# Performance work log

Hardware: AMD Instinct MI355X
Metric: run time of the kernel (lower is better)

## Reference

```python
import jax, jax.numpy as jnp
import numpy as np

K = 8               # top-k frequencies
PRED_LEN = 96       # prediction_length
LOW_FREQ = 1        # low_frequency cutoff (drops DC)


def setup_inputs() -> dict:
    key = jax.random.key(0)
    x = jax.random.normal(key, (32, 2048, 64), dtype=jnp.float32)
    return {"x": x}


def reference(x):
    b, t, d = x.shape
    x_freq = jnp.fft.rfft(x, axis=1)                 # (b, t//2+1, d) complex
    freqs = jnp.fft.rfftfreq(t).astype(x.dtype)
    if t % 2 == 0:
        x_freq = x_freq[:, LOW_FREQ:-1]              # drop DC and Nyquist
        f = freqs[LOW_FREQ:-1]
    else:
        x_freq = x_freq[:, LOW_FREQ:]
        f = freqs[LOW_FREQ:]

    # top-k over frequency dim (axis=1), independently per (b, d)
    mag = jnp.abs(x_freq)                            # (b, F, d)
    _, idx = jax.lax.top_k(jnp.moveaxis(mag, 1, 2), K)  # (b, d, K), sorted desc
    idx = jnp.moveaxis(idx, 1, 2)                    # (b, K, d)
    x_k = jnp.take_along_axis(x_freq, idx, axis=1)   # (b, K, d) complex
    f_k = f[idx]                                     # (b, K, d)

    # extrapolate: add conjugate (negative) frequencies, then cos-sum
    x2 = jnp.concatenate([x_k, jnp.conj(x_k)], axis=1)  # (b, 2K, d)
    f2 = jnp.concatenate([f_k, -f_k], axis=1)           # (b, 2K, d)
    t_val = jnp.arange(t + PRED_LEN, dtype=x.dtype)     # (T,)
    amp = jnp.abs(x2) / t                               # (b, 2K, d)
    phase = jnp.angle(x2)                               # (b, 2K, d)
    # (b, 2K, T, d) broadcast intermediate, reduced over freq axis
    x_time = amp[:, :, None, :] * jnp.cos(
        2.0 * np.float32(np.pi) * f2[:, :, None, :] * t_val[None, None, :, None]
        + phase[:, :, None, :]
    )
    return x_time.sum(axis=1)                        # (b, t+PRED_LEN, d)
```

## Files before the change

### kernel.cpp

```cpp
#include <hip/hip_runtime.h>
#include <math.h>

#define BB 32
#define TT 2048
#define DD 64
#define PRED 96
#define TP (TT + PRED)
#define KTOP 8
#define MARGIN 8e-4f
#define PI_D 3.14159265358979323846
#define XT2_BYTES ((size_t)BB * 32 * TT * sizeof(float2))

__device__ __forceinline__ int br6(int l) { return (int)(__brev((unsigned)l) >> 26); }
static constexpr int BR3[8] = {0,4,2,6,1,5,3,7};
static constexpr float C32T[16] = {
    1.0f, 0.98078528040323044913f, 0.92387953251128675613f, 0.83146961230254523708f,
    0.70710678118654752440f, 0.55557023301960222474f, 0.38268343236508977173f, 0.19509032201612826785f,
    0.0f, -0.19509032201612826785f, -0.38268343236508977173f, -0.55557023301960222474f,
    -0.70710678118654752440f, -0.83146961230254523708f, -0.92387953251128675613f, -0.98078528040323044913f};
static constexpr float S32T[16] = {
    0.0f, 0.19509032201612826785f, 0.38268343236508977173f, 0.55557023301960222474f,
    0.70710678118654752440f, 0.83146961230254523708f, 0.92387953251128675613f, 0.98078528040323044913f,
    1.0f, 0.98078528040323044913f, 0.92387953251128675613f, 0.83146961230254523708f,
    0.70710678118654752440f, 0.55557023301960222474f, 0.38268343236508977173f, 0.19509032201612826785f};

__device__ __forceinline__ float2 ctw(float2 a, int m) {
    const float rev = (float)m * (1.0f / 2048.0f);
    const float c = __builtin_amdgcn_cosf(rev);
    const float s = __builtin_amdgcn_sinf(rev);
    return make_float2(a.x * c + a.y * s, a.y * c - a.x * s);
}

__global__ __launch_bounds__(256) void transpose_kernel(const float* __restrict__ x,
                                                        float2* __restrict__ xt2) {
    __shared__ float tl[64 * 68];
    const int tid = threadIdx.x;
    const int bid = blockIdx.x;
    const int b   = bid >> 5;
    const int t0  = (bid & 31) * 64;

    const float4* xr = (const float4*)(x + ((size_t)b * TT + t0) * DD);
    {
        const int r = tid >> 2, c = tid & 3;
        #pragma unroll
        for (int j = 0; j < 4; ++j) {
            const float4 f = xr[r * 16 + c + 4 * j];
            *(float4*)&tl[r * 68 + (c + 4 * j) * 4] = f;
        }
    }
    __syncthreads();

    {
        const int dp = tid >> 3, c = tid & 7;
        float2* orow = xt2 + ((size_t)b * 32 + dp) * TT + t0;
        #pragma unroll
        for (int j = 0; j < 4; ++j) {
            const int t = 16 * j + 2 * c;
            float4 o;
            o.x = tl[t * 68 + 2 * dp];
            o.y = tl[t * 68 + 2 * dp + 1];
            o.z = tl[(t + 1) * 68 + 2 * dp];
            o.w = tl[(t + 1) * 68 + 2 * dp + 1];
            *(float4*)&orow[t] = o;
        }
    }
}

#define EXB(wvi,pi) ((wvi) * 1152 + (pi) * 18)
#define SRE(a) POOL[4608 + (a)]
#define SIM(a) POOL[6720 + (a)]

template<bool XT>
__global__ __launch_bounds__(256, 4) void fused_kernel(const float* __restrict__ x,
                                                       const float2* __restrict__ xt2,
                                                       float* __restrict__ out) {
    __shared__ float POOL[8832];
    __shared__ int   coefK[2][KTOP];
    __shared__ float coefR[2][KTOP], coefI[2][KTOP];

    const int t    = threadIdx.x;
    const int wv   = t >> 6, p = t & 63;
    const int bid  = blockIdx.x;
    const int xcd  = bid & 7;
    const int idx  = bid >> 3;
    const int b    = ((idx >> 3) << 1) | (xcd >> 2);
    const int dp   = ((xcd & 3) << 3) | (idx & 7);

    const float2* xp = XT ? (xt2 + ((size_t)b * 32 + dp) * TT) : (const float2*)0;
    const float2* xv = (const float2*)x;
    const size_t xbase = (size_t)b * TT * (DD / 2) + dp;
    const int br2wv = ((wv & 1) << 1) | ((wv >> 1) & 1);
    const int rl = 4 * br6(p) + br2wv;

    float2 v[8];
    #pragma unroll
    for (int i = 0; i < 8; ++i) {
        const int n = 256 * BR3[i] + rl;
        v[i] = XT ? xp[n] : xv[xbase + (size_t)n * (DD / 2)];
    }

    #pragma unroll
    for (int s = 1; s <= 3; ++s) {
        const int m = 1 << s, half = m >> 1, stepw = 32 >> s;
        #pragma unroll
        for (int g = 0; g < 8; g += m) {
            #pragma unroll
            for (int j = 0; j < half; ++j) {
                const float c = C32T[j * stepw], sn = S32T[j * stepw];
                const int i0 = g + j, i1 = i0 + half;
                const float tr = c * v[i1].x + sn * v[i1].y;
                const float ti = c * v[i1].y - sn * v[i1].x;
                v[i1] = make_float2(v[i0].x - tr, v[i0].y - ti);
                v[i0] = make_float2(v[i0].x + tr, v[i0].y + ti);
            }
        }
    }

    #pragma unroll
    for (int q = 1; q < 8; ++q) v[q] = ctw(v[q], (rl * q) & (TT - 1));

    #pragma unroll
    for (int s = 1; s <= 6; ++s) {
        const int half = 1 << (s - 1);
        const float rev = (float)(p & (half - 1)) / (float)(1 << s);
        const float wc  = __builtin_amdgcn_cosf(rev);
        const float wsn = __builtin_amdgcn_sinf(rev);
        const bool  hi  = (p & half) != 0;
        #pragma unroll
        for (int q = 0; q < 8; ++q) {
            float2 pv;
            pv.x = __shfl_xor(v[q].x, half, 64);
            pv.y = __shfl_xor(v[q].y, half, 64);
            const float2 bsv = hi ? v[q] : pv;
            const float2 asv = hi ? pv : v[q];
            const float tr = wc * bsv.x + wsn * bsv.y;
            const float ti = wc * bsv.y - wsn * bsv.x;
            v[q] = hi ? make_float2(asv.x - tr, asv.y - ti)
                      : make_float2(asv.x + tr, asv.y + ti);
        }
    }

    {
        const int exw = EXB(wv, p);
        #pragma unroll
        for (int q = 0; q < 8; ++q) *(float2*)&POOL[exw + 2 * q] = v[q];
    }
    __syncthreads();
    {
        const int exr = EXB(wv ^ 1, p);
        const float rev7 = (float)p * (1.0f / 128.0f);
        const float c7 = __builtin_amdgcn_cosf(rev7);
        const float s7 = __builtin_amdgcn_sinf(rev7);
        const bool hi7 = (wv & 1) != 0;
        #pragma unroll
        for (int q = 0; q < 8; ++q) {
            const float2 pv = *(const float2*)&POOL[exr + 2 * q];
            const float2 bsv = hi7 ? v[q] : pv;
            const float2 asv = hi7 ? pv : v[q];
            const float tr = c7 * bsv.x + s7 * bsv.y;
            const float ti = c7 * bsv.y - s7 * bsv.x;
            v[q] = hi7 ? make_float2(asv.x - tr, asv.y - ti)
                       : make_float2(asv.x + tr, asv.y + ti);
        }
    }
    __syncthreads();

    {
        const int exw = EXB(wv, p);
        #pragma unroll
        for (int q = 0; q < 8; ++q) *(float2*)&POOL[exw + 2 * q] = v[q];
    }
    __syncthreads();
    {
        const int exr = EXB(wv ^ 2, p);
        const float rev8 = (float)(64 * (wv & 1) + p) * (1.0f / 256.0f);
        const float c8 = __builtin_amdgcn_cosf(rev8);
        const float s8 = __builtin_amdgcn_sinf(rev8);
        const bool hi8 = ((wv >> 1) & 1) != 0;
        const int kb = 512 * wv + 8 * p;
        #pragma unroll
        for (int q = 0; q < 8; ++q) {
            const float2 pv = *(const float2*)&POOL[exr + 2 * q];
            const float2 bsv = hi8 ? v[q] : pv;
            const float2 asv = hi8 ? pv : v[q];
            const float tr = c8 * bsv.x + s8 * bsv.y;
            const float ti = c8 * bsv.y - s8 * bsv.x;
            const float re = hi8 ? (asv.x - tr) : (asv.x + tr);
            const float im = hi8 ? (asv.y - ti) : (asv.y + ti);
            const int k = kb + q, a = k + (k >> 5);
            SRE(a) = re;
            SIM(a) = im;
        }
    }
    __syncthreads();

    if (wv < 2) {
        const int w = wv;
        unsigned A[16];
        #pragma unroll
        for (int q = 0; q < 16; ++q) {
            const int k = 16 * p + q;
            unsigned kk = 0u;
            if (k != 0) {
                const int a1 = k + (k >> 5);
                const int pk = TT - k, a2 = pk + (pk >> 5);
                const float zr = SRE(a1), zi = SIM(a1);
                const float yr = SRE(a2), yi = SIM(a2);
                float cr, ci;
                if (w == 0) { cr = 0.5f * (zr + yr); ci = 0.5f * (zi - yi); }
                else        { cr = 0.5f * (zi + yi); ci = 0.5f * (yr - zr); }
                const float mg = cr * cr + ci * ci;
                kk = (__float_as_uint(mg) & 0xFFFFF800u) | (unsigned)(2047 - k);
            }
            A[q] = kk;
        }

        #pragma unroll
        for (int sz = 2; sz <= 16; sz <<= 1) {
            #pragma unroll
            for (int d = sz >> 1; d > 0; d >>= 1) {
                #pragma unroll
                for (int i2 = 0; i2 < 16; ++i2) {
                    const int j2i = i2 ^ d;
                    if (j2i > i2) {
                        const bool desc = ((i2 & sz) == 0);
                        const unsigned a = A[i2], b2 = A[j2i];
                        const unsigned mx = a > b2 ? a : b2, mn = a > b2 ? b2 : a;
                        A[i2] = desc ? mx : mn;  A[j2i] = desc ? mn : mx;
                    }
                }
            }
        }
        #pragma unroll
        for (int off = 1; off <= 32; off <<= 1) {
            unsigned Bv[16];
            #pragma unroll
            for (int i2 = 0; i2 < 16; ++i2)
                Bv[i2] = (unsigned)__shfl_xor((int)A[i2], off, 64);
            #pragma unroll
            for (int i2 = 0; i2 < 16; ++i2) {
                const unsigned o = Bv[15 - i2];
                A[i2] = A[i2] > o ? A[i2] : o;
            }
            #pragma unroll
            for (int d = 8; d > 0; d >>= 1) {
                #pragma unroll
                for (int i2 = 0; i2 < 16; ++i2) {
                    if ((i2 & d) == 0) {
                        const int j2i = i2 + d;
                        const unsigned a = A[i2], b2 = A[j2i];
                        A[i2] = a > b2 ? a : b2;  A[j2i] = a > b2 ? b2 : a;
                    }
                }
            }
        }

        const float m8f = __uint_as_float(A[7] & 0xFFFFF800u);
        unsigned bandmask = 0u;
        #pragma unroll
        for (int r = 0; r < 16; ++r) {
            const float mr = __uint_as_float(A[r] & 0xFFFFF800u);
            if (fabsf(mr - m8f) <= MARGIN * m8f) bandmask |= (1u << r);
        }
        const int flg = (bandmask != (1u << 7)) ? 1 : 0;

        unsigned myk = 0u;
        #pragma unroll
        for (int i2 = 0; i2 < 16; ++i2) myk = (p == i2) ? A[i2] : myk;
        const int kcand = 2047 - (int)(myk & 0x7FFu);

        if (!flg && p < KTOP) {
            const int k = kcand, a1 = k + (k >> 5), pk = TT - k, a2 = pk + (pk >> 5);
            const float zr = SRE(a1), zi = SIM(a1);
            const float yr = SRE(a2), yi = SIM(a2);
            float cr, ci;
            if (w == 0) { cr = 0.5f * (zr + yr); ci = 0.5f * (zi - yi); }
            else        { cr = 0.5f * (zi + yi); ci = 0.5f * (yr - zr); }
            coefK[w][p] = k;
            coefR[w][p] = cr * (2.0f / (float)TT);
            coefI[w][p] = ci * (2.0f / (float)TT);
        }

        if (flg) {
            float sv[32];
            #pragma unroll
            for (int m2 = 0; m2 < 32; ++m2) {
                if (XT) {
                    const float2 s2 = xp[p + 64 * m2];
                    sv[m2] = (w == 0) ? s2.x : s2.y;
                } else {
                    const float* xs = x + (size_t)b * TT * DD + 2 * dp + w;
                    sv[m2] = xs[(size_t)(p + 64 * m2) * DD];
                }
            }
            const double thA = -2.0 * PI_D * (double)p / 64.0;
            const double thB = -2.0 * PI_D * (double)p / (double)TT;
            const double wac = cos(thA), was = sin(thA);
            const double wbc = cos(thB), wbs = sin(thB);

            const unsigned bm = bandmask;
            const int lo = (int)__builtin_ctz(bm);
            double myM = 0.0, myR = 0.0, myI = 0.0;
            for (int r = 0; r < 16; ++r) {
                if (!((bm >> r) & 1u)) continue;
                const int kr = __shfl(kcand, r, 64);
                double ar = 0.0, ai = 0.0;
                for (int m2 = 0; m2 < 32; ++m2) {
                    const int n  = p + 64 * m2;
                    const int mm = (n * kr) & (TT - 1);
                    const double qc  = __shfl(wac, mm >> 5, 64);
                    const double qs  = __shfl(was, mm >> 5, 64);
                    const double rc2 = __shfl(wbc, mm & 31, 64);
                    const double rs2 = __shfl(wbs, mm & 31, 64);
                    const double wr = qc * rc2 - qs * rs2;
                    const double wi = qc * rs2 + qs * rc2;
                    ar = fma((double)sv[m2], wr, ar);
                    ai = fma((double)sv[m2], wi, ai);
                }
                #pragma unroll
                for (int off = 32; off; off >>= 1) {
                    ar += __shfl_xor(ar, off, 64);
                    ai += __shfl_xor(ai, off, 64);
                }
                if (p == r) { myM = ar * ar + ai * ai; myR = ar; myI = ai; }
            }
            const int h16 = p & 15;
            const double selfM = __shfl(myM, h16, 64);
            const int    selfK = __shfl(kcand, h16, 64);
            int rb = 0;
            for (int r2 = 0; r2 < 16; ++r2) {
                if (!((bm >> r2) & 1u)) continue;
                const double om = __shfl(myM, r2, 64);
                const int    ok = __shfl(kcand, r2, 64);
                if (r2 != h16 && (om > selfM || (om == selfM && ok < selfK))) ++rb;
            }
            const int isband = (int)((bm >> h16) & 1u);
            const int rank = isband ? (lo + rb) : h16;
            if (p < 16 && rank < KTOP) {
                coefK[w][rank] = kcand;
                if (isband) {
                    coefR[w][rank] = (float)(myR * (2.0 / (double)TT));
                    coefI[w][rank] = (float)(myI * (2.0 / (double)TT));
                } else {
                    const int k = kcand, a1 = k + (k >> 5), pk = TT - k, a2 = pk + (pk >> 5);
                    const float zr = SRE(a1), zi = SIM(a1);
                    const float yr = SRE(a2), yi = SIM(a2);
                    float cr, ci;
                    if (w == 0) { cr = 0.5f * (zr + yr); ci = 0.5f * (zi - yi); }
                    else        { cr = 0.5f * (zi + yi); ci = 0.5f * (yr - zr); }
                    coefR[w][rank] = cr * (2.0f / (float)TT);
                    coefI[w][rank] = ci * (2.0f / (float)TT);
                }
            }
        }
    }
    __syncthreads();

    const int d2 = t & 1, tq = t >> 1;
    int   kc[KTOP];
    float fr[KTOP], fi[KTOP], pc[KTOP], ps[KTOP], rc[KTOP], rs[KTOP];
    #pragma unroll
    for (int pp = 0; pp < KTOP; ++pp) {
        kc[pp] = coefK[d2][pp];
        fr[pp] = coefR[d2][pp];
        fi[pp] = coefI[d2][pp];
        const int j0 = (kc[pp] * tq) & (TT - 1);
        const float rv0 = (float)j0 * (1.0f / 2048.0f);
        pc[pp] = __builtin_amdgcn_cosf(rv0);
        ps[pp] = __builtin_amdgcn_sinf(rv0);
        const int jr = (kc[pp] * 128) & (TT - 1);
        const float rvr = (float)jr * (1.0f / 2048.0f);
        rc[pp] = __builtin_amdgcn_cosf(rvr);
        rs[pp] = __builtin_amdgcn_sinf(rvr);
    }
    float* ob = out + (size_t)b * TP * DD + 2 * dp + d2;
    #pragma unroll 2
    for (int m = 0; m < 17; ++m) {
        const int tv = tq + 128 * m;
        float acc = 0.0f;
        #pragma unroll
        for (int pp = 0; pp < KTOP; ++pp) acc += fr[pp] * pc[pp] - fi[pp] * ps[pp];
        if (tv < TP) ob[(size_t)tv * DD] = acc;
        #pragma unroll
        for (int pp = 0; pp < KTOP; ++pp) {
            const float nc = pc[pp] * rc[pp] - ps[pp] * rs[pp];
            const float ns = pc[pp] * rs[pp] + ps[pp] * rc[pp];
            pc[pp] = nc; ps[pp] = ns;
        }
    }
}

extern "C" void kernel_launch(void* const* d_in, const int* in_sizes, int n_in,
                              void* d_out, int out_size, void* d_ws, size_t ws_size,
                              hipStream_t stream) {
    const float* x = (const float*)d_in[0];
    float* out = (float*)d_out;
    (void)in_sizes; (void)n_in; (void)out_size;

    if (d_ws != nullptr && ws_size >= XT2_BYTES) {
        float2* xt2 = (float2*)d_ws;
        transpose_kernel<<<BB * 32, 256, 0, stream>>>(x, xt2);
        fused_kernel<true><<<BB * 32, 256, 0, stream>>>(x, xt2, out);
    } else {
        fused_kernel<false><<<BB * 32, 256, 0, stream>>>(x, nullptr, out);
    }
}
```

Measured before the change: 103.7 us.

## Split fused kernel into FFT-select and coalesced synthesis kernels via workspace

```diff
diff --git a/kernel.cpp b/kernel.cpp
--- a/kernel.cpp
+++ b/kernel.cpp
@@ -10,6 +10,8 @@
 #define MARGIN 8e-4f
 #define PI_D 3.14159265358979323846
 #define XT2_BYTES ((size_t)BB * 32 * TT * sizeof(float2))
+#define GCOEF_BYTES ((size_t)BB * DD * KTOP * sizeof(float4))
+#define WS_NEED (XT2_BYTES + GCOEF_BYTES)
 
 __device__ __forceinline__ int br6(int l) { return (int)(__brev((unsigned)l) >> 26); }
 static constexpr int BR3[8] = {0,4,2,6,1,5,3,7};
@@ -49,7 +51,6 @@
         }
     }
     __syncthreads();
-
     {
         const int dp = tid >> 3, c = tid & 7;
         float2* orow = xt2 + ((size_t)b * 32 + dp) * TT + t0;
@@ -70,34 +71,23 @@
 #define SRE(a) POOL[4608 + (a)]
 #define SIM(a) POOL[6720 + (a)]
 
-template<bool XT>
-__global__ __launch_bounds__(256, 4) void fused_kernel(const float* __restrict__ x,
-                                                       const float2* __restrict__ xt2,
-                                                       float* __restrict__ out) {
+__global__ __launch_bounds__(256, 2) void fft_select_kernel(const float2* __restrict__ xt2,
+                                                            float4* __restrict__ gcoef) {
     __shared__ float POOL[8832];
-    __shared__ int   coefK[2][KTOP];
-    __shared__ float coefR[2][KTOP], coefI[2][KTOP];
-
     const int t    = threadIdx.x;
     const int wv   = t >> 6, p = t & 63;
     const int bid  = blockIdx.x;
-    const int xcd  = bid & 7;
-    const int idx  = bid >> 3;
-    const int b    = ((idx >> 3) << 1) | (xcd >> 2);
-    const int dp   = ((xcd & 3) << 3) | (idx & 7);
-
-    const float2* xp = XT ? (xt2 + ((size_t)b * 32 + dp) * TT) : (const float2*)0;
-    const float2* xv = (const float2*)x;
-    const size_t xbase = (size_t)b * TT * (DD / 2) + dp;
+    const int b    = bid >> 5;
+    const int dp   = bid & 31;
+
+    const float2* xp = xt2 + ((size_t)b * 32 + dp) * TT;
     const int br2wv = ((wv & 1) << 1) | ((wv >> 1) & 1);
     const int rl = 4 * br6(p) + br2wv;
 
     float2 v[8];
     #pragma unroll
-    for (int i = 0; i < 8; ++i) {
-        const int n = 256 * BR3[i] + rl;
-        v[i] = XT ? xp[n] : xv[xbase + (size_t)n * (DD / 2)];
-    }
+    for (int i = 0; i < 8; ++i)
+        v[i] = xp[256 * BR3[i] + rl];
 
     #pragma unroll
     for (int s = 1; s <= 3; ++s) {
@@ -115,7 +105,6 @@
             }
         }
     }
-
     #pragma unroll
     for (int q = 1; q < 8; ++q) v[q] = ctw(v[q], (rl * q) & (TT - 1));
 
@@ -165,6 +154,338 @@
     }
     __syncthreads();
 
+    {
+        const int exw = EXB(wv, p);
+        #pragma unroll
+        for (int q = 0; q < 8; ++q) *(float2*)&POOL[exw + 2 * q] = v[q];
+    }
+    __syncthreads();
+    {
+        const int exr = EXB(wv ^ 2, p);
+        const float rev8 = (float)(64 * (wv & 1) + p) * (1.0f / 256.0f);
+        const float c8 = __builtin_amdgcn_cosf(rev8);
+        const float s8 = __builtin_amdgcn_sinf(rev8);
+        const bool hi8 = ((wv >> 1) & 1) != 0;
+        const int kb = 512 * wv + 8 * p;
+        #pragma unroll
+        for (int q = 0; q < 8; ++q) {
+            const float2 pv = *(const float2*)&POOL[exr + 2 * q];
+            const float2 bsv = hi8 ? v[q] : pv;
+            const float2 asv = hi8 ? pv : v[q];
+            const float tr = c8 * bsv.x + s8 * bsv.y;
+            const float ti = c8 * bsv.y - s8 * bsv.x;
+            const float re = hi8 ? (asv.x - tr) : (asv.x + tr);
+            const float im = hi8 ? (asv.y - ti) : (asv.y + ti);
+            const int k = kb + q, a = k + (k >> 5);
+            SRE(a) = re;
+            SIM(a) = im;
+        }
+    }
+    __syncthreads();
+
+    if (wv >= 2) return;
+
+    const int w = wv;
+    float4* gout = gcoef + ((size_t)b * DD + 2 * dp + w) * KTOP;
+    unsigned A[16];
+    #pragma unroll
+    for (int q = 0; q < 16; ++q) {
+        const int k = 16 * p + q;
+        unsigned kk = 0u;
+        if (k != 0) {
+            const int a1 = k + (k >> 5);
+            const int pk = TT - k, a2 = pk + (pk >> 5);
+            const float zr = SRE(a1), zi = SIM(a1);
+            const float yr = SRE(a2), yi = SIM(a2);
+            float cr, ci;
+            if (w == 0) { cr = 0.5f * (zr + yr); ci = 0.5f * (zi - yi); }
+            else        { cr = 0.5f * (zi + yi); ci = 0.5f * (yr - zr); }
+            const float mg = cr * cr + ci * ci;
+            kk = (__float_as_uint(mg) & 0xFFFFF800u) | (unsigned)(2047 - k);
+        }
+        A[q] = kk;
+    }
+    #pragma unroll
+    for (int sz = 2; sz <= 16; sz <<= 1) {
+        #pragma unroll
+        for (int d = sz >> 1; d > 0; d >>= 1) {
+            #pragma unroll
+            for (int i2 = 0; i2 < 16; ++i2) {
+                const int j2i = i2 ^ d;
+                if (j2i > i2) {
+                    const bool desc = ((i2 & sz) == 0);
+                    const unsigned a = A[i2], b2 = A[j2i];
+                    const unsigned mx = a > b2 ? a : b2, mn = a > b2 ? b2 : a;
+                    A[i2] = desc ? mx : mn;  A[j2i] = desc ? mn : mx;
+                }
+            }
+        }
+    }
+    #pragma unroll
+    for (int off = 1; off <= 32; off <<= 1) {
+        unsigned Bv[16];
+        #pragma unroll
+        for (int i2 = 0; i2 < 16; ++i2)
+            Bv[i2] = (unsigned)__shfl_xor((int)A[i2], off, 64);
+        #pragma unroll
+        for (int i2 = 0; i2 < 16; ++i2) {
+            const unsigned o = Bv[15 - i2];
+            A[i2] = A[i2] > o ? A[i2] : o;
+        }
+        #pragma unroll
+        for (int d = 8; d > 0; d >>= 1) {
+            #pragma unroll
+            for (int i2 = 0; i2 < 16; ++i2) {
+                if ((i2 & d) == 0) {
+                    const int j2i = i2 + d;
+                    const unsigned a = A[i2], b2 = A[j2i];
+                    A[i2] = a > b2 ? a : b2;  A[j2i] = a > b2 ? b2 : a;
+                }
+            }
+        }
+    }
+
+    const float m8f = __uint_as_float(A[7] & 0xFFFFF800u);
+    unsigned bandmask = 0u;
+    #pragma unroll
+    for (int r = 0; r < 16; ++r) {
+        const float mr = __uint_as_float(A[r] & 0xFFFFF800u);
+        if (fabsf(mr - m8f) <= MARGIN * m8f) bandmask |= (1u << r);
+    }
+    const int flg = (bandmask != (1u << 7)) ? 1 : 0;
+
+    unsigned myk = 0u;
+    #pragma unroll
+    for (int i2 = 0; i2 < 16; ++i2) myk = (p == i2) ? A[i2] : myk;
+    const int kcand = 2047 - (int)(myk & 0x7FFu);
+
+    if (!flg && p < KTOP) {
+        const int k = kcand, a1 = k + (k >> 5), pk = TT - k, a2 = pk + (pk >> 5);
+        const float zr = SRE(a1), zi = SIM(a1);
+        const float yr = SRE(a2), yi = SIM(a2);
+        float cr, ci;
+        if (w == 0) { cr = 0.5f * (zr + yr); ci = 0.5f * (zi - yi); }
+        else        { cr = 0.5f * (zi + yi); ci = 0.5f * (yr - zr); }
+        gout[p] = make_float4(cr * (2.0f / (float)TT), ci * (2.0f / (float)TT),
+                              (float)k, 0.0f);
+    }
+
+    if (flg) {
+        float sv[32];
+        #pragma unroll
+        for (int m2 = 0; m2 < 32; ++m2) {
+            const float2 s2 = xp[p + 64 * m2];
+            sv[m2] = (w == 0) ? s2.x : s2.y;
+        }
+        const double thA = -2.0 * PI_D * (double)p / 64.0;
+        const double thB = -2.0 * PI_D * (double)p / (double)TT;
+        const double wac = cos(thA), was = sin(thA);
+        const double wbc = cos(thB), wbs = sin(thB);
+
+        const unsigned bm = bandmask;
+        const int lo = (int)__builtin_ctz(bm);
+        double myM = 0.0, myR = 0.0, myI = 0.0;
+        for (int r = 0; r < 16; ++r) {
+            if (!((bm >> r) & 1u)) continue;
+            const int kr = __shfl(kcand, r, 64);
+            double ar = 0.0, ai = 0.0;
+            for (int m2 = 0; m2 < 32; ++m2) {
+                const int n  = p + 64 * m2;
+                const int mm = (n * kr) & (TT - 1);
+                const double qc  = __shfl(wac, mm >> 5, 64);
+                const double qs  = __shfl(was, mm >> 5, 64);
+                const double rc2 = __shfl(wbc, mm & 31, 64);
+                const double rs2 = __shfl(wbs, mm & 31, 64);
+                const double wr = qc * rc2 - qs * rs2;
+                const double wi = qc * rs2 + qs * rc2;
+                ar = fma((double)sv[m2], wr, ar);
+                ai = fma((double)sv[m2], wi, ai);
+            }
+            #pragma unroll
+            for (int off = 32; off; off >>= 1) {
+                ar += __shfl_xor(ar, off, 64);
+                ai += __shfl_xor(ai, off, 64);
+            }
+            if (p == r) { myM = ar * ar + ai * ai; myR = ar; myI = ai; }
+        }
+        const int h16 = p & 15;
+        const double selfM = __shfl(myM, h16, 64);
+        const int    selfK = __shfl(kcand, h16, 64);
+        int rb = 0;
+        for (int r2 = 0; r2 < 16; ++r2) {
+            if (!((bm >> r2) & 1u)) continue;
+            const double om = __shfl(myM, r2, 64);
+            const int    ok = __shfl(kcand, r2, 64);
+            if (r2 != h16 && (om > selfM || (om == selfM && ok < selfK))) ++rb;
+        }
+        const int isband = (int)((bm >> h16) & 1u);
+        const int rank = isband ? (lo + rb) : h16;
+        if (p < 16 && rank < KTOP) {
+            if (isband) {
+                gout[rank] = make_float4((float)(myR * (2.0 / (double)TT)),
+                                         (float)(myI * (2.0 / (double)TT)),
+                                         (float)kcand, 0.0f);
+            } else {
+                const int k = kcand, a1 = k + (k >> 5), pk = TT - k, a2 = pk + (pk >> 5);
+                const float zr = SRE(a1), zi = SIM(a1);
+                const float yr = SRE(a2), yi = SIM(a2);
+                float cr, ci;
+                if (w == 0) { cr = 0.5f * (zr + yr); ci = 0.5f * (zi - yi); }
+                else        { cr = 0.5f * (zi + yi); ci = 0.5f * (yr - zr); }
+                gout[rank] = make_float4(cr * (2.0f / (float)TT),
+                                         ci * (2.0f / (float)TT), (float)k, 0.0f);
+            }
+        }
+    }
+}
+
+__global__ __launch_bounds__(256, 4) void synth_kernel(const float4* __restrict__ gcoef,
+                                                       float* __restrict__ out) {
+    __shared__ float4 gcf[64 * 9];
+    __shared__ float  TL[67 * 64];
+    const int tid = threadIdx.x;
+    const int bid = blockIdx.x;
+    const int b   = bid >> 5;
+    const int t0  = (bid & 31) * 67;
+
+    {
+        const float4* gsrc = gcoef + (size_t)b * DD * KTOP;
+        #pragma unroll
+        for (int j = 0; j < 2; ++j) {
+            const int i = tid + 256 * j;
+            const float4 g = gsrc[i];
+            gcf[(i >> 3) * 9 + (i & 7)] = g;
+        }
+    }
+    __syncthreads();
+
+    const int d = tid & 63, tq = tid >> 6;
+    float fr[KTOP], fi[KTOP], pc[KTOP], ps[KTOP], rc[KTOP], rs[KTOP];
+    #pragma unroll
+    for (int k = 0; k < KTOP; ++k) {
+        const float4 g = gcf[d * 9 + k];
+        fr[k] = g.x; fi[k] = g.y;
+        const int kc = (int)g.z;
+        const int j0 = (kc * (t0 + tq)) & (TT - 1);
+        pc[k] = __builtin_amdgcn_cosf((float)j0 * (1.0f / 2048.0f));
+        ps[k] = __builtin_amdgcn_sinf((float)j0 * (1.0f / 2048.0f));
+        const int jr = (kc * 4) & (TT - 1);
+        rc[k] = __builtin_amdgcn_cosf((float)jr * (1.0f / 2048.0f));
+        rs[k] = __builtin_amdgcn_sinf((float)jr * (1.0f / 2048.0f));
+    }
+    #pragma unroll 2
+    for (int m = 0; m < 17; ++m) {
+        const int tloc = tq + 4 * m;
+        float acc = 0.0f;
+        #pragma unroll
+        for (int k = 0; k < KTOP; ++k) acc += fr[k] * pc[k] - fi[k] * ps[k];
+        if (tloc < 67) TL[tloc * 64 + d] = acc;
+        #pragma unroll
+        for (int k = 0; k < KTOP; ++k) {
+            const float nc = pc[k] * rc[k] - ps[k] * rs[k];
+            const float ns = pc[k] * rs[k] + ps[k] * rc[k];
+            pc[k] = nc; ps[k] = ns;
+        }
+    }
+    __syncthreads();
+
+    float* ob = out + ((size_t)b * TP + t0) * DD;
+    #pragma unroll
+    for (int it = 0; it < 5; ++it) {
+        const int idx = it * 256 + tid;
+        if (idx < 1072) {
+            const int row = idx >> 4, q = idx & 15;
+            *(float4*)&ob[(size_t)row * DD + 4 * q] = *(const float4*)&TL[row * 64 + 4 * q];
+        }
+    }
+}
+
+__global__ __launch_bounds__(256, 4) void mono_kernel(const float* __restrict__ x,
+                                                      float* __restrict__ out) {
+    __shared__ float POOL[8832];
+    __shared__ int   coefK[2][KTOP];
+    __shared__ float coefR[2][KTOP], coefI[2][KTOP];
+
+    const int t    = threadIdx.x;
+    const int wv   = t >> 6, p = t & 63;
+    const int bid  = blockIdx.x;
+    const int xcd  = bid & 7;
+    const int idx  = bid >> 3;
+    const int b    = ((idx >> 3) << 1) | (xcd >> 2);
+    const int dp   = ((xcd & 3) << 3) | (idx & 7);
+
+    const float2* xv = (const float2*)x;
+    const size_t xbase = (size_t)b * TT * (DD / 2) + dp;
+    const int br2wv = ((wv & 1) << 1) | ((wv >> 1) & 1);
+    const int rl = 4 * br6(p) + br2wv;
+
+    float2 v[8];
+    #pragma unroll
+    for (int i = 0; i < 8; ++i)
+        v[i] = xv[xbase + (size_t)(256 * BR3[i] + rl) * (DD / 2)];
+
+    #pragma unroll
+    for (int s = 1; s <= 3; ++s) {
+        const int m = 1 << s, half = m >> 1, stepw = 32 >> s;
+        #pragma unroll
+        for (int g = 0; g < 8; g += m) {
+            #pragma unroll
+            for (int j = 0; j < half; ++j) {
+                const float c = C32T[j * stepw], sn = S32T[j * stepw];
+                const int i0 = g + j, i1 = i0 + half;
+                const float tr = c * v[i1].x + sn * v[i1].y;
+                const float ti = c * v[i1].y - sn * v[i1].x;
+                v[i1] = make_float2(v[i0].x - tr, v[i0].y - ti);
+                v[i0] = make_float2(v[i0].x + tr, v[i0].y + ti);
+            }
+        }
+    }
+    #pragma unroll
+    for (int q = 1; q < 8; ++q) v[q] = ctw(v[q], (rl * q) & (TT - 1));
+    #pragma unroll
+    for (int s = 1; s <= 6; ++s) {
+        const int half = 1 << (s - 1);
+        const float rev = (float)(p & (half - 1)) / (float)(1 << s);
+        const float wc  = __builtin_amdgcn_cosf(rev);
+        const float wsn = __builtin_amdgcn_sinf(rev);
+        const bool  hi  = (p & half) != 0;
+        #pragma unroll
+        for (int q = 0; q < 8; ++q) {
+            float2 pv;
+            pv.x = __shfl_xor(v[q].x, half, 64);
+            pv.y = __shfl_xor(v[q].y, half, 64);
+            const float2 bsv = hi ? v[q] : pv;
+            const float2 asv = hi ? pv : v[q];
+            const float tr = wc * bsv.x + wsn * bsv.y;
+            const float ti = wc * bsv.y - wsn * bsv.x;
+            v[q] = hi ? make_float2(asv.x - tr, asv.y - ti)
+                      : make_float2(asv.x + tr, asv.y + ti);
+        }
+    }
+    {
+        const int exw = EXB(wv, p);
+        #pragma unroll
+        for (int q = 0; q < 8; ++q) *(float2*)&POOL[exw + 2 * q] = v[q];
+    }
+    __syncthreads();
+    {
+        const int exr = EXB(wv ^ 1, p);
+        const float rev7 = (float)p * (1.0f / 128.0f);
+        const float c7 = __builtin_amdgcn_cosf(rev7);
+        const float s7 = __builtin_amdgcn_sinf(rev7);
+        const bool hi7 = (wv & 1) != 0;
+        #pragma unroll
+        for (int q = 0; q < 8; ++q) {
+            const float2 pv = *(const float2*)&POOL[exr + 2 * q];
+            const float2 bsv = hi7 ? v[q] : pv;
+            const float2 asv = hi7 ? pv : v[q];
+            const float tr = c7 * bsv.x + s7 * bsv.y;
+            const float ti = c7 * bsv.y - s7 * bsv.x;
+            v[q] = hi7 ? make_float2(asv.x - tr, asv.y - ti)
+                       : make_float2(asv.x + tr, asv.y + ti);
+        }
+    }
+    __syncthreads();
     {
         const int exw = EXB(wv, p);
         #pragma unroll
@@ -214,7 +535,6 @@
             }
             A[q] = kk;
         }
-
         #pragma unroll
         for (int sz = 2; sz <= 16; sz <<= 1) {
             #pragma unroll
@@ -254,7 +574,6 @@
                 }
             }
         }
-
         const float m8f = __uint_as_float(A[7] & 0xFFFFF800u);
         unsigned bandmask = 0u;
         #pragma unroll
@@ -263,7 +582,6 @@
             if (fabsf(mr - m8f) <= MARGIN * m8f) bandmask |= (1u << r);
         }
         const int flg = (bandmask != (1u << 7)) ? 1 : 0;
-
         unsigned myk = 0u;
         #pragma unroll
         for (int i2 = 0; i2 < 16; ++i2) myk = (p == i2) ? A[i2] : myk;
@@ -280,24 +598,16 @@
             coefR[w][p] = cr * (2.0f / (float)TT);
             coefI[w][p] = ci * (2.0f / (float)TT);
         }
-
         if (flg) {
             float sv[32];
-            #pragma unroll
-            for (int m2 = 0; m2 < 32; ++m2) {
-                if (XT) {
-                    const float2 s2 = xp[p + 64 * m2];
-                    sv[m2] = (w == 0) ? s2.x : s2.y;
-                } else {
-                    const float* xs = x + (size_t)b * TT * DD + 2 * dp + w;
-                    sv[m2] = xs[(size_t)(p + 64 * m2) * DD];
-                }
-            }
+            const float* xs = x + (size_t)b * TT * DD + 2 * dp + w;
+            #pragma unroll
+            for (int m2 = 0; m2 < 32; ++m2)
+                sv[m2] = xs[(size_t)(p + 64 * m2) * DD];
             const double thA = -2.0 * PI_D * (double)p / 64.0;
             const double thB = -2.0 * PI_D * (double)p / (double)TT;
             const double wac = cos(thA), was = sin(thA);
             const double wbc = cos(thB), wbs = sin(thB);
-
             const unsigned bm = bandmask;
             const int lo = (int)__builtin_ctz(bm);
             double myM = 0.0, myR = 0.0, myI = 0.0;
@@ -357,21 +667,18 @@
     __syncthreads();
 
     const int d2 = t & 1, tq = t >> 1;
-    int   kc[KTOP];
     float fr[KTOP], fi[KTOP], pc[KTOP], ps[KTOP], rc[KTOP], rs[KTOP];
     #pragma unroll
     for (int pp = 0; pp < KTOP; ++pp) {
-        kc[pp] = coefK[d2][pp];
+        const int kc = coefK[d2][pp];
         fr[pp] = coefR[d2][pp];
         fi[pp] = coefI[d2][pp];
-        const int j0 = (kc[pp] * tq) & (TT - 1);
-        const float rv0 = (float)j0 * (1.0f / 2048.0f);
-        pc[pp] = __builtin_amdgcn_cosf(rv0);
-        ps[pp] = __builtin_amdgcn_sinf(rv0);
-        const int jr = (kc[pp] * 128) & (TT - 1);
-        const float rvr = (float)jr * (1.0f / 2048.0f);
-        rc[pp] = __builtin_amdgcn_cosf(rvr);
-        rs[pp] = __builtin_amdgcn_sinf(rvr);
+        const int j0 = (kc * tq) & (TT - 1);
+        pc[pp] = __builtin_amdgcn_cosf((float)j0 * (1.0f / 2048.0f));
+        ps[pp] = __builtin_amdgcn_sinf((float)j0 * (1.0f / 2048.0f));
+        const int jr = (kc * 128) & (TT - 1);
+        rc[pp] = __builtin_amdgcn_cosf((float)jr * (1.0f / 2048.0f));
+        rs[pp] = __builtin_amdgcn_sinf((float)jr * (1.0f / 2048.0f));
     }
     float* ob = out + (size_t)b * TP * DD + 2 * dp + d2;
     #pragma unroll 2
@@ -397,11 +704,13 @@
     float* out = (float*)d_out;
     (void)in_sizes; (void)n_in; (void)out_size;
 
-    if (d_ws != nullptr && ws_size >= XT2_BYTES) {
-        float2* xt2 = (float2*)d_ws;
+    if (d_ws != nullptr && ws_size >= WS_NEED) {
+        float2* xt2   = (float2*)d_ws;
+        float4* gcoef = (float4*)((char*)d_ws + XT2_BYTES);
         transpose_kernel<<<BB * 32, 256, 0, stream>>>(x, xt2);
-        fused_kernel<true><<<BB * 32, 256, 0, stream>>>(x, xt2, out);
+        fft_select_kernel<<<BB * 32, 256, 0, stream>>>(xt2, gcoef);
+        synth_kernel<<<BB * 32, 256, 0, stream>>>(gcoef, out);
     } else {
-        fused_kernel<false><<<BB * 32, 256, 0, stream>>>(x, nullptr, out);
+        mono_kernel<<<BB * 32, 256, 0, stream>>>(x, out);
     }
 }
```

Result: no change. 105.2 us (+1.5%).
